# Kernel tuning notes

Measured on AMD Instinct MI355X. Metric: run time of the kernel, lower is better.

Reference implementation:

```python
import jax, jax.numpy as jnp
import numpy as np

E, D_IN, H1, H2 = 10, 784, 256, 64


def setup_inputs() -> dict:
    key = jax.random.key(0)
    ks = jax.random.split(key, 11)
    s = lambda fan_in: 1.0 / np.sqrt(fan_in)
    return {
        "x": jax.random.normal(ks[0], (65536, D_IN), dtype=jnp.float32),
        # stacked expert weights (E experts of Linear layers)
        "W1": jax.random.uniform(ks[1], (E, D_IN, H1), jnp.float32, -s(D_IN), s(D_IN)),
        "b1": jax.random.uniform(ks[2], (E, H1), jnp.float32, -s(D_IN), s(D_IN)),
        "W2": jax.random.uniform(ks[3], (E, H1, H2), jnp.float32, -s(H1), s(H1)),
        "b2": jax.random.uniform(ks[4], (E, H2), jnp.float32, -s(H1), s(H1)),
        "W3": jax.random.uniform(ks[5], (E, H2), jnp.float32, -s(H2), s(H2)),  # [E,64,1] squeezed
        "b3": jax.random.uniform(ks[6], (E,), jnp.float32, -s(H2), s(H2)),
        # gate: 784 -> 256 -> E
        "Wg1": jax.random.uniform(ks[7], (D_IN, H1), jnp.float32, -s(D_IN), s(D_IN)),
        "bg1": jax.random.uniform(ks[8], (H1,), jnp.float32, -s(D_IN), s(D_IN)),
        "Wg2": jax.random.uniform(ks[9], (H1, E), jnp.float32, -s(H1), s(H1)),
        "bg2": jax.random.uniform(ks[10], (E,), jnp.float32, -s(H1), s(H1)),
    }


def reference(x, W1, b1, W2, b2, W3, b3, Wg1, bg1, Wg2, bg2):
    # dense all-experts MLP stack, batched over experts as grouped GEMMs
    h = jax.nn.relu(jnp.einsum("bi,eih->beh", x, W1) + b1)        # [B,E,256]
    h = jax.nn.relu(jnp.einsum("beh,ehk->bek", h, W2) + b2)        # [B,E,64]
    expert_outputs = jnp.einsum("bek,ek->be", h, W3) + b3          # [B,E]
    g = jax.nn.relu(x @ Wg1 + bg1)
    gate_scores = jax.nn.softmax(g @ Wg2 + bg2, axis=-1)           # [B,E]
    output = gate_scores * expert_outputs                          # [B,E]
    return (output, gate_scores, expert_outputs)
```

## Files before the change

### kernel.cpp

```cpp
#include <hip/hip_runtime.h>
#include <hip/hip_bf16.h>
#include <stdint.h>

#define BTOT   65536
#define DIN    784
#define K1P    800
#define NH1    256
#define NH2    64
#define NEXP   10
#define BM     64
#define NKS1   25
#define NKS2   9

#define XS_B      102400
#define H_OFF     XS_B
#define H_B       36864
#define EXP2_OFF  (H_OFF + H_B)
#define W3S_OFF   (EXP2_OFF + BM * NEXP * 2 * 4)
#define B3S_OFF   (W3S_OFF + NEXP * NH2 * 4)
#define LDS_TOTAL (B3S_OFF + 64)

typedef short s16x8  __attribute__((ext_vector_type(8)));
typedef float f32x4  __attribute__((ext_vector_type(4)));
typedef float f32x16 __attribute__((ext_vector_type(16)));

__device__ __forceinline__ short bf16b(float v) {
    __bf16 b = (__bf16)v;
    return __builtin_bit_cast(short, b);
}

__global__ void prep_w1(const float* __restrict__ W1, const float* __restrict__ b1,
                        const float* __restrict__ Wg1, const float* __restrict__ bg1,
                        __bf16* __restrict__ dst) {
    int t = blockIdx.x * 256 + threadIdx.x;
    int lane = t & 63;
    int rr = t >> 6;
    int kh = rr & 1;
    int ks = (rr >> 1) % 25;
    int nb = ((rr >> 1) / 25) % 8;
    int e  = (rr >> 1) / 200;
    int n  = nb * 32 + (lane & 31);
    int k0 = ks * 32 + kh * 16 + (lane >> 5) * 8;
    const float* src  = (e < NEXP) ? (W1 + (size_t)e * DIN * NH1) : Wg1;
    const float* bias = (e < NEXP) ? (b1 + e * NH1) : bg1;
    s16x8 o;
    #pragma unroll
    for (int j = 0; j < 8; ++j) {
        int k = k0 + j;
        float v = (k < DIN) ? src[(size_t)k * NH1 + n]
                            : ((k == DIN) ? bias[n] : 0.f);
        o[j] = bf16b(v);
    }
    *(s16x8*)((short*)dst + (size_t)t * 8) = o;
}

__global__ void prep_w2(const float* __restrict__ W2, const float* __restrict__ b2,
                        __bf16* __restrict__ dst) {
    int t = blockIdx.x * 256 + threadIdx.x;
    int lane = t & 63;
    int rr = t >> 6;
    int kh = rr & 1;
    int ks = (rr >> 1) % 9;
    int jb = ((rr >> 1) / 9) & 1;
    int e  = (rr >> 1) / 18;
    int n  = jb * 32 + (lane & 31);
    int k0 = ks * 32 + kh * 16 + (lane >> 5) * 8;
    s16x8 o;
    #pragma unroll
    for (int j = 0; j < 8; ++j) {
        int k = k0 + j;
        float v = (k < NH1) ? W2[((size_t)e * NH1 + k) * NH2 + n]
                            : ((k == NH1) ? b2[e * NH2 + n] : 0.f);
        o[j] = bf16b(v);
    }
    *(s16x8*)((short*)dst + (size_t)t * 8) = o;
}

__global__ void prep_wg2(const float* __restrict__ Wg2, const float* __restrict__ bg2,
                         __bf16* __restrict__ dst) {
    int t = blockIdx.x * 256 + threadIdx.x;
    if (t >= 9 * 2 * 64) return;
    int lane = t & 63;
    int rr = t >> 6;
    int kh = rr & 1;
    int ks = rr >> 1;
    int n  = lane & 31;
    int k0 = ks * 32 + kh * 16 + (lane >> 5) * 8;
    s16x8 o;
    #pragma unroll
    for (int j = 0; j < 8; ++j) {
        int k = k0 + j;
        float v = 0.f;
        if (n < NEXP) {
            if (k < NH1)       v = Wg2[(size_t)k * NEXP + n];
            else if (k == NH1) v = bg2[n];
        }
        o[j] = bf16b(v);
    }
    *(s16x8*)((short*)dst + (size_t)t * 8) = o;
}

#define L1A_PF(S, T)                                                          \
    { _Pragma("unroll") for (int mt = 0; mt < 2; ++mt)                        \
        _Pragma("unroll") for (int kh = 0; kh < 2; ++kh)                      \
            a[S][mt][kh] = *(const s16x8*)(pA + ((mt * 25 + (T)) * 2 + kh) * 1024); }

#define L1W_PF(S, T, PW)                                                      \
    { _Pragma("unroll") for (int nt = 0; nt < 2; ++nt)                        \
        _Pragma("unroll") for (int kh = 0; kh < 2; ++kh)                      \
            w[S][nt][kh] = *(const s16x8*)((PW) + nt * 51200 + ((T) * 2 + kh) * 1024); }

#define L1_PF(S, T) L1A_PF(S, T) L1W_PF(S, T, pW)

#define L1_MMA(S)                                                             \
    { _Pragma("unroll") for (int nt = 0; nt < 2; ++nt)                        \
        _Pragma("unroll") for (int mt = 0; mt < 2; ++mt)                      \
            _Pragma("unroll") for (int kh = 0; kh < 2; ++kh)                  \
                acc[nt][mt] = __builtin_amdgcn_mfma_f32_32x32x16_bf16(        \
                    w[S][nt][kh], a[S][mt][kh], acc[nt][mt], 0, 0, 0); }

#define L2_PF(S, T)                                                           \
    { _Pragma("unroll") for (int kh = 0; kh < 2; ++kh) {                      \
        hfr[S][kh] = *(const s16x8*)(pH + ((T) * 2 + kh) * 1024);             \
        v2[S][kh]  = *(const s16x8*)(pV + ((T) * 2 + kh) * 1024); } }

#define L2_MMA(S)                                                             \
    { _Pragma("unroll") for (int kh = 0; kh < 2; ++kh)                        \
        acc2 = __builtin_amdgcn_mfma_f32_32x32x16_bf16(                       \
            v2[S][kh], hfr[S][kh], acc2, 0, 0, 0); }

__global__ void __launch_bounds__(256, 1)
moe_fused(const float* __restrict__ x, const float* __restrict__ W3,
          const float* __restrict__ b3, const __bf16* __restrict__ w1t,
          const __bf16* __restrict__ w2t, const __bf16* __restrict__ wg2t,
          float* __restrict__ out)
{
    extern __shared__ char lds[];
    char*  xsb   = lds;
    char*  hb    = lds + H_OFF;
    float* expl2 = (float*)(lds + EXP2_OFF);
    float* w3s   = (float*)(lds + W3S_OFF);
    float* b3s   = (float*)(lds + B3S_OFF);

    const int tid  = threadIdx.x;
    const int lane = tid & 63;
    const int wave = tid >> 6;
    const int rl   = lane & 31;
    const int hi   = lane >> 5;
    const int row0 = blockIdx.x * BM;
    const char* w1c = (const char*)w1t;

    const char* pA = xsb + lane * 16;
    const char* pW = w1c + (size_t)(wave * 2) * 51200 + lane * 16;

    s16x8 w[3][2][2], a[3][2][2];
    L1W_PF(0, 0, pW) L1W_PF(1, 1, pW) L1W_PF(2, 2, pW)

    {
        const float* xg = x + (size_t)row0 * DIN;
        #pragma unroll 4
        for (int i = 0; i < 49; ++i) {
            int idx = tid + i * 256;
            int r = idx / 196, c = (idx % 196) * 4;
            float4 v = *(const float4*)(xg + (size_t)r * DIN + c);
            int ks = c >> 5, kin = c & 31;
            int kh = kin >> 4, hw = (kin >> 3) & 1, j = c & 7;
            uint2 wv; short* p = (short*)&wv;
            p[0] = bf16b(v.x); p[1] = bf16b(v.y);
            p[2] = bf16b(v.z); p[3] = bf16b(v.w);
            *(uint2*)(xsb + ((((r >> 5) * 25 + ks) * 2 + kh) * 2 + hw) * 512
                          + (r & 31) * 16 + j * 2) = wv;
        }
        for (int i = tid; i < 64 * 4; i += 256) {
            int r = i >> 2, g = i & 3;
            int hw = g >> 1, j0 = (g & 1) * 4;
            uint2 wv = {0u, 0u};
            if (g == 0) ((short*)&wv)[0] = bf16b(1.f);
            *(uint2*)(xsb + ((((r >> 5) * 25 + 24) * 2 + 1) * 2 + hw) * 512
                          + (r & 31) * 16 + j0 * 2) = wv;
        }
        for (int i = tid; i < 2 * 1024; i += 256) {
            int mb = i >> 10, q = i & 1023;
            short v = (q < 256 && (q & 7) == 0) ? bf16b(1.f) : (short)0;
            *(short*)(hb + (mb * 9 + 8) * 2048 + q * 2) = v;
        }
        for (int i = tid; i < NEXP * NH2; i += 256) w3s[i] = W3[i];
        if (tid < NEXP) b3s[tid] = b3[tid];
    }
    __syncthreads();

    L1A_PF(0, 0) L1A_PF(1, 1) L1A_PF(2, 2)

    #pragma unroll 1
    for (int e = 0; e <= NEXP; ++e) {
        const char* pWe = w1c + (size_t)(e * 8 + wave * 2) * 51200 + lane * 16;
        #define pW pWe

        f32x16 acc[2][2];
        #pragma unroll
        for (int nt = 0; nt < 2; ++nt)
            #pragma unroll
            for (int mt = 0; mt < 2; ++mt)
                #pragma unroll
                for (int q = 0; q < 16; ++q) acc[nt][mt][q] = 0.f;

        #pragma unroll 1
        for (int T = 0; T < 7; ++T) {
            const int t3 = 3 * T;
            L1_MMA(0) L1_PF(0, t3 + 3)
            L1_MMA(1) L1_PF(1, t3 + 4)
            L1_MMA(2) L1_PF(2, t3 + 5)
        }
        L1_MMA(0) L1_PF(0, 24)
        L1_MMA(1)
        L1_MMA(2)
        #undef pW

        const int mb2 = wave >> 1, jb = wave & 1;
        const char* pH = hb + mb2 * 18432 + lane * 16;
        const char* pV = (const char*)w2t + (size_t)(e * 2 + jb) * 18432 + lane * 16;
        s16x8 v2[3][2], hfr[3][2];
        if (e < NEXP) {
            #pragma unroll
            for (int p = 0; p < 3; ++p)
                #pragma unroll
                for (int kh = 0; kh < 2; ++kh)
                    v2[p][kh] = *(const s16x8*)(pV + (p * 2 + kh) * 1024);
        }
        L1_MMA(0)

        if (e < NEXP) {
            const char* pWn = pWe + 8 * 51200;
            L1W_PF(0, 0, pWn) L1W_PF(1, 1, pWn) L1W_PF(2, 2, pWn)
            L1A_PF(0, 0) L1A_PF(1, 1) L1A_PF(2, 2)
        }

        __syncthreads();
        #pragma unroll
        for (int mt = 0; mt < 2; ++mt)
            #pragma unroll
            for (int nt = 0; nt < 2; ++nt) {
                const int ks2 = wave * 2 + nt;
                #pragma unroll
                for (int q = 0; q < 4; ++q) {
                    uint2 wv; short* p = (short*)&wv;
                    #pragma unroll
                    for (int r2 = 0; r2 < 4; ++r2)
                        p[r2] = bf16b(fmaxf(acc[nt][mt][q * 4 + r2], 0.f));
                    *(uint2*)(hb + ((mt * 9 + ks2) * 2 + (q >> 1)) * 1024
                                 + (q & 1) * 512 + rl * 16 + hi * 8) = wv;
                }
            }
        __syncthreads();

        if (e < NEXP) {
            f32x16 acc2;
            #pragma unroll
            for (int q = 0; q < 16; ++q) acc2[q] = 0.f;
            #pragma unroll
            for (int kh = 0; kh < 2; ++kh)
                hfr[0][kh] = *(const s16x8*)(pH + (0 * 2 + kh) * 1024);
            #pragma unroll
            for (int kh = 0; kh < 2; ++kh)
                hfr[1][kh] = *(const s16x8*)(pH + (1 * 2 + kh) * 1024);
            #pragma unroll
            for (int kh = 0; kh < 2; ++kh)
                hfr[2][kh] = *(const s16x8*)(pH + (2 * 2 + kh) * 1024);

            #pragma unroll 1
            for (int T = 0; T < 2; ++T) {
                const int t3 = 3 * T;
                L2_MMA(0) L2_PF(0, t3 + 3)
                L2_MMA(1) L2_PF(1, t3 + 4)
                L2_MMA(2) L2_PF(2, t3 + 5)
            }
            L2_MMA(0) L2_MMA(1) L2_MMA(2)

            float part = 0.f;
            const float* w3p = w3s + e * NH2 + jb * 32 + 4 * hi;
            #pragma unroll
            for (int q = 0; q < 4; ++q) {
                f32x4 w3v = *(const f32x4*)(w3p + 8 * q);
                #pragma unroll
                for (int r2 = 0; r2 < 4; ++r2)
                    part += fmaxf(acc2[q * 4 + r2], 0.f) * w3v[r2];
            }
            part += __shfl_xor(part, 32, 64);
            if (hi == 0)
                expl2[(mb2 * 32 + rl) * (NEXP * 2) + e * 2 + jb] = part;
        } else if (wave < 2) {
            const int mbg = wave;
            const char* pHg = hb + mbg * 18432 + lane * 16;
            const char* pG  = (const char*)wg2t + lane * 16;
            f32x16 acc3;
            #pragma unroll
            for (int q = 0; q < 16; ++q) acc3[q] = 0.f;
            {
                s16x8 v2[3][2], hfr[3][2];
                const char* pH = pHg;
                const char* pV = pG;
                L2_PF(0, 0) L2_PF(1, 1) L2_PF(2, 2)
                #define acc2 acc3
                #pragma unroll 1
                for (int T = 0; T < 2; ++T) {
                    const int t3 = 3 * T;
                    L2_MMA(0) L2_PF(0, t3 + 3)
                    L2_MMA(1) L2_PF(1, t3 + 4)
                    L2_MMA(2) L2_PF(2, t3 + 5)
                }
                L2_MMA(0) L2_MMA(1) L2_MMA(2)
                #undef acc2
            }
            const int m = mbg * 32 + rl;
            float mx = -1e30f;
            float lv[16];
            #pragma unroll
            for (int q = 0; q < 4; ++q)
                #pragma unroll
                for (int r2 = 0; r2 < 4; ++r2) {
                    int j = r2 + 8 * q + 4 * hi;
                    int rg = q * 4 + r2;
                    lv[rg] = (j < NEXP) ? acc3[rg] : -1e30f;
                    mx = fmaxf(mx, lv[rg]);
                }
            mx = fmaxf(mx, __shfl_xor(mx, 32, 64));
            float s = 0.f;
            float pv[16];
            #pragma unroll
            for (int rg = 0; rg < 16; ++rg) {
                pv[rg] = (lv[rg] > -1e29f) ? __expf(lv[rg] - mx) : 0.f;
                s += pv[rg];
            }
            s += __shfl_xor(s, 32, 64);
            const float inv = 1.f / s;
            #pragma unroll
            for (int q = 0; q < 4; ++q)
                #pragma unroll
                for (int r2 = 0; r2 < 4; ++r2) {
                    int j = r2 + 8 * q + 4 * hi;
                    if (j < NEXP) {
                        float g  = pv[q * 4 + r2] * inv;
                        float eo = expl2[m * (NEXP * 2) + j * 2]
                                 + expl2[m * (NEXP * 2) + j * 2 + 1]
                                 + b3s[j];
                        size_t o = (size_t)(row0 + m) * NEXP + j;
                        out[o] = g * eo;
                        out[(size_t)BTOT * NEXP + o] = g;
                        out[(size_t)2 * BTOT * NEXP + o] = eo;
                    }
                }
        }
    }
}

extern "C" void kernel_launch(void* const* d_in, const int* in_sizes, int n_in,
                              void* d_out, int out_size, void* d_ws, size_t ws_size,
                              hipStream_t stream) {
    (void)in_sizes; (void)n_in; (void)out_size; (void)ws_size;
    const float* x   = (const float*)d_in[0];
    const float* W1  = (const float*)d_in[1];
    const float* b1  = (const float*)d_in[2];
    const float* W2  = (const float*)d_in[3];
    const float* b2  = (const float*)d_in[4];
    const float* W3  = (const float*)d_in[5];
    const float* b3  = (const float*)d_in[6];
    const float* Wg1 = (const float*)d_in[7];
    const float* bg1 = (const float*)d_in[8];
    const float* Wg2 = (const float*)d_in[9];
    const float* bg2 = (const float*)d_in[10];

    __bf16* w1t  = (__bf16*)d_ws;
    __bf16* w2t  = w1t + (size_t)11 * 8 * 25 * 2 * 64 * 8;
    __bf16* wg2t = w2t + (size_t)10 * 2 * 9 * 2 * 64 * 8;

    hipFuncSetAttribute((const void*)moe_fused,
                        hipFuncAttributeMaxDynamicSharedMemorySize, LDS_TOTAL);

    prep_w1<<<1100, 256, 0, stream>>>(W1, b1, Wg1, bg1, w1t);
    prep_w2<<<90, 256, 0, stream>>>(W2, b2, w2t);
    prep_wg2<<<5, 256, 0, stream>>>(Wg2, bg2, wg2t);
    moe_fused<<<BTOT / BM, 256, LDS_TOTAL, stream>>>(x, W3, b3, w1t, w2t, wg2t,
                                                     (float*)d_out);
}
```

Baseline: 349.6 us.

## Process two experts per layer-1 pass to reuse x fragments across experts

The layer-1 loop now computes two experts at once. Each x fragment loaded from LDS feeds MFMAs for both experts' weight tiles, which halves the LDS reads of A per expert and doubles the independent MFMA chains. The gate network runs as a separate final single-expert pass. In exchange the prefetch depth drops from three stages to two and the kernel holds twice as many accumulators, which raises register pressure on a kernel already running one block per CU.

```diff
diff --git a/kernel.cpp b/kernel.cpp
--- a/kernel.cpp
+++ b/kernel.cpp
@@ -100,24 +100,46 @@
     *(s16x8*)((short*)dst + (size_t)t * 8) = o;
 }
 
-#define L1A_PF(S, T)                                                          \
+#define PFA(S, T)                                                             \
     { _Pragma("unroll") for (int mt = 0; mt < 2; ++mt)                        \
         _Pragma("unroll") for (int kh = 0; kh < 2; ++kh)                      \
             a[S][mt][kh] = *(const s16x8*)(pA + ((mt * 25 + (T)) * 2 + kh) * 1024); }
 
-#define L1W_PF(S, T, PW)                                                      \
+#define PFW(S, E, T, PW)                                                      \
     { _Pragma("unroll") for (int nt = 0; nt < 2; ++nt)                        \
         _Pragma("unroll") for (int kh = 0; kh < 2; ++kh)                      \
-            w[S][nt][kh] = *(const s16x8*)((PW) + nt * 51200 + ((T) * 2 + kh) * 1024); }
-
-#define L1_PF(S, T) L1A_PF(S, T) L1W_PF(S, T, pW)
-
-#define L1_MMA(S)                                                             \
+            w[S][E][nt][kh] = *(const s16x8*)((PW) + nt * 51200                \
+                                              + ((T) * 2 + kh) * 1024); }
+
+#define PMMA(S, E)                                                            \
     { _Pragma("unroll") for (int nt = 0; nt < 2; ++nt)                        \
         _Pragma("unroll") for (int mt = 0; mt < 2; ++mt)                      \
             _Pragma("unroll") for (int kh = 0; kh < 2; ++kh)                  \
-                acc[nt][mt] = __builtin_amdgcn_mfma_f32_32x32x16_bf16(        \
-                    w[S][nt][kh], a[S][mt][kh], acc[nt][mt], 0, 0, 0); }
+                acc[E][nt][mt] = __builtin_amdgcn_mfma_f32_32x32x16_bf16(     \
+                    w[S][E][nt][kh], a[S][mt][kh], acc[E][nt][mt], 0, 0, 0); }
+
+#define ZACC(E)                                                               \
+    { _Pragma("unroll") for (int nt = 0; nt < 2; ++nt)                        \
+        _Pragma("unroll") for (int mt = 0; mt < 2; ++mt)                      \
+            _Pragma("unroll") for (int q = 0; q < 16; ++q)                    \
+                acc[E][nt][mt][q] = 0.f; }
+
+#define HWRITE(E)                                                             \
+    { _Pragma("unroll") for (int mt = 0; mt < 2; ++mt)                        \
+        _Pragma("unroll") for (int nt = 0; nt < 2; ++nt) {                    \
+            const int ks2 = wave * 2 + nt;                                    \
+            _Pragma("unroll") for (int q = 0; q < 4; ++q) {                   \
+                uint2 wv; short* p = (short*)&wv;                             \
+                _Pragma("unroll") for (int r2 = 0; r2 < 4; ++r2)              \
+                    p[r2] = bf16b(fmaxf(acc[E][nt][mt][q * 4 + r2], 0.f));    \
+                *(uint2*)(hb + ((mt * 9 + ks2) * 2 + (q >> 1)) * 1024         \
+                             + (q & 1) * 512 + rl * 16 + hi * 8) = wv;        \
+            } } }
+
+#define PF_V2(PV)                                                             \
+    { _Pragma("unroll") for (int p = 0; p < 3; ++p)                           \
+        _Pragma("unroll") for (int kh = 0; kh < 2; ++kh)                      \
+            v2[p][kh] = *(const s16x8*)((PV) + (p * 2 + kh) * 1024); }
 
 #define L2_PF(S, T)                                                           \
     { _Pragma("unroll") for (int kh = 0; kh < 2; ++kh) {                      \
@@ -128,6 +150,36 @@
     { _Pragma("unroll") for (int kh = 0; kh < 2; ++kh)                        \
         acc2 = __builtin_amdgcn_mfma_f32_32x32x16_bf16(                       \
             v2[S][kh], hfr[S][kh], acc2, 0, 0, 0); }
+
+#define DO_L2(EV, PV)                                                         \
+    {                                                                         \
+        const char* pV = (PV);                                                \
+        f32x16 acc2;                                                          \
+        _Pragma("unroll") for (int q = 0; q < 16; ++q) acc2[q] = 0.f;         \
+        _Pragma("unroll") for (int kh = 0; kh < 2; ++kh)                      \
+            hfr[0][kh] = *(const s16x8*)(pH + (0 * 2 + kh) * 1024);           \
+        _Pragma("unroll") for (int kh = 0; kh < 2; ++kh)                      \
+            hfr[1][kh] = *(const s16x8*)(pH + (1 * 2 + kh) * 1024);           \
+        _Pragma("unroll") for (int kh = 0; kh < 2; ++kh)                      \
+            hfr[2][kh] = *(const s16x8*)(pH + (2 * 2 + kh) * 1024);           \
+        _Pragma("unroll 1") for (int T = 0; T < 2; ++T) {                     \
+            const int t3 = 3 * T;                                             \
+            L2_MMA(0) L2_PF(0, t3 + 3)                                        \
+            L2_MMA(1) L2_PF(1, t3 + 4)                                        \
+            L2_MMA(2) L2_PF(2, t3 + 5)                                        \
+        }                                                                     \
+        L2_MMA(0) L2_MMA(1) L2_MMA(2)                                         \
+        float part = 0.f;                                                     \
+        const float* w3p = w3s + (EV) * NH2 + jb * 32 + 4 * hi;               \
+        _Pragma("unroll") for (int q = 0; q < 4; ++q) {                       \
+            f32x4 w3v = *(const f32x4*)(w3p + 8 * q);                         \
+            _Pragma("unroll") for (int r2 = 0; r2 < 4; ++r2)                  \
+                part += fmaxf(acc2[q * 4 + r2], 0.f) * w3v[r2];               \
+        }                                                                     \
+        part += __shfl_xor(part, 32, 64);                                     \
+        if (hi == 0)                                                          \
+            expl2[(mb2 * 32 + rl) * (NEXP * 2) + (EV) * 2 + jb] = part;       \
+    }
 
 __global__ void __launch_bounds__(256, 1)
 moe_fused(const float* __restrict__ x, const float* __restrict__ W3,
@@ -151,10 +203,18 @@
     const char* w1c = (const char*)w1t;
 
     const char* pA = xsb + lane * 16;
-    const char* pW = w1c + (size_t)(wave * 2) * 51200 + lane * 16;
-
-    s16x8 w[3][2][2], a[3][2][2];
-    L1W_PF(0, 0, pW) L1W_PF(1, 1, pW) L1W_PF(2, 2, pW)
+    const int mb2 = wave >> 1, jb = wave & 1;
+    const char* pH = hb + mb2 * 18432 + lane * 16;
+
+    s16x8 w[2][2][2][2];
+    s16x8 a[2][2][2];
+    s16x8 v2[3][2], hfr[3][2];
+    {
+        const char* pW0 = w1c + (size_t)(wave * 2) * 51200 + lane * 16;
+        const char* pW1 = pW0 + 8 * 51200;
+        PFW(0, 0, 0, pW0) PFW(1, 0, 1, pW0)
+        PFW(0, 1, 0, pW1) PFW(1, 1, 1, pW1)
+    }
 
     {
         const float* xg = x + (size_t)row0 * DIN;
@@ -189,84 +249,81 @@
     }
     __syncthreads();
 
-    L1A_PF(0, 0) L1A_PF(1, 1) L1A_PF(2, 2)
+    PFA(0, 0) PFA(1, 1)
+
+    f32x16 acc[2][2][2];
 
     #pragma unroll 1
-    for (int e = 0; e <= NEXP; ++e) {
-        const char* pWe = w1c + (size_t)(e * 8 + wave * 2) * 51200 + lane * 16;
-        #define pW pWe
-
-        f32x16 acc[2][2];
+    for (int p5 = 0; p5 < 5; ++p5) {
+        const int e0 = 2 * p5;
+        const char* pW0 = w1c + (size_t)(e0 * 8 + wave * 2) * 51200 + lane * 16;
+        const char* pW1 = pW0 + 8 * 51200;
+
+        ZACC(0) ZACC(1)
+
+        #pragma unroll 1
+        for (int T = 0; T < 11; ++T) {
+            const int t2 = 2 * T;
+            PMMA(0, 0) PMMA(0, 1)
+            PFW(0, 0, t2 + 2, pW0) PFW(0, 1, t2 + 2, pW1) PFA(0, t2 + 2)
+            PMMA(1, 0) PMMA(1, 1)
+            PFW(1, 0, t2 + 3, pW0) PFW(1, 1, t2 + 3, pW1) PFA(1, t2 + 3)
+        }
+        PMMA(0, 0) PMMA(0, 1)
+        PFW(0, 0, 24, pW0) PFW(0, 1, 24, pW1) PFA(0, 24)
+        PMMA(1, 0) PMMA(1, 1)
+        PMMA(0, 0) PMMA(0, 1)
+
+        PF_V2((const char*)w2t + (size_t)(e0 * 2 + jb) * 18432 + lane * 16)
+        {
+            const char* pW0n = pW0 + 16 * 51200;
+            const char* pW1n = (p5 < 4) ? (pW1 + 16 * 51200) : pW0n;
+            PFW(0, 0, 0, pW0n) PFW(1, 0, 1, pW0n)
+            PFW(0, 1, 0, pW1n) PFW(1, 1, 1, pW1n)
+            PFA(0, 0) PFA(1, 1)
+        }
+
+        __syncthreads();
+        HWRITE(0)
+        __syncthreads();
+        DO_L2(e0, (const char*)w2t + (size_t)(e0 * 2 + jb) * 18432 + lane * 16)
+        PF_V2((const char*)w2t + (size_t)((e0 + 1) * 2 + jb) * 18432 + lane * 16)
+        __syncthreads();
+        HWRITE(1)
+        __syncthreads();
+        DO_L2(e0 + 1, (const char*)w2t + (size_t)((e0 + 1) * 2 + jb) * 18432 + lane * 16)
+    }
+
+    {
+        const char* pWg = w1c + (size_t)(10 * 8 + wave * 2) * 51200 + lane * 16;
+        ZACC(0)
+        #pragma unroll 1
+        for (int T = 0; T < 11; ++T) {
+            const int t2 = 2 * T;
+            PMMA(0, 0) PFW(0, 0, t2 + 2, pWg) PFA(0, t2 + 2)
+            PMMA(1, 0) PFW(1, 0, t2 + 3, pWg) PFA(1, t2 + 3)
+        }
+        PMMA(0, 0) PFW(0, 0, 24, pWg) PFA(0, 24)
+        PMMA(1, 0)
+        PMMA(0, 0)
+
+        __syncthreads();
+        HWRITE(0)
+        __syncthreads();
+    }
+
+    if (wave < 2) {
+        const int mbg = wave;
+        const char* pHg = hb + mbg * 18432 + lane * 16;
+        const char* pG  = (const char*)wg2t + lane * 16;
+        f32x16 acc3;
         #pragma unroll
-        for (int nt = 0; nt < 2; ++nt)
-            #pragma unroll
-            for (int mt = 0; mt < 2; ++mt)
-                #pragma unroll
-                for (int q = 0; q < 16; ++q) acc[nt][mt][q] = 0.f;
-
-        #pragma unroll 1
-        for (int T = 0; T < 7; ++T) {
-            const int t3 = 3 * T;
-            L1_MMA(0) L1_PF(0, t3 + 3)
-            L1_MMA(1) L1_PF(1, t3 + 4)
-            L1_MMA(2) L1_PF(2, t3 + 5)
-        }
-        L1_MMA(0) L1_PF(0, 24)
-        L1_MMA(1)
-        L1_MMA(2)
-        #undef pW
-
-        const int mb2 = wave >> 1, jb = wave & 1;
-        const char* pH = hb + mb2 * 18432 + lane * 16;
-        const char* pV = (const char*)w2t + (size_t)(e * 2 + jb) * 18432 + lane * 16;
-        s16x8 v2[3][2], hfr[3][2];
-        if (e < NEXP) {
-            #pragma unroll
-            for (int p = 0; p < 3; ++p)
-                #pragma unroll
-                for (int kh = 0; kh < 2; ++kh)
-                    v2[p][kh] = *(const s16x8*)(pV + (p * 2 + kh) * 1024);
-        }
-        L1_MMA(0)
-
-        if (e < NEXP) {
-            const char* pWn = pWe + 8 * 51200;
-            L1W_PF(0, 0, pWn) L1W_PF(1, 1, pWn) L1W_PF(2, 2, pWn)
-            L1A_PF(0, 0) L1A_PF(1, 1) L1A_PF(2, 2)
-        }
-
-        __syncthreads();
-        #pragma unroll
-        for (int mt = 0; mt < 2; ++mt)
-            #pragma unroll
-            for (int nt = 0; nt < 2; ++nt) {
-                const int ks2 = wave * 2 + nt;
-                #pragma unroll
-                for (int q = 0; q < 4; ++q) {
-                    uint2 wv; short* p = (short*)&wv;
-                    #pragma unroll
-                    for (int r2 = 0; r2 < 4; ++r2)
-                        p[r2] = bf16b(fmaxf(acc[nt][mt][q * 4 + r2], 0.f));
-                    *(uint2*)(hb + ((mt * 9 + ks2) * 2 + (q >> 1)) * 1024
-                                 + (q & 1) * 512 + rl * 16 + hi * 8) = wv;
-                }
-            }
-        __syncthreads();
-
-        if (e < NEXP) {
-            f32x16 acc2;
-            #pragma unroll
-            for (int q = 0; q < 16; ++q) acc2[q] = 0.f;
-            #pragma unroll
-            for (int kh = 0; kh < 2; ++kh)
-                hfr[0][kh] = *(const s16x8*)(pH + (0 * 2 + kh) * 1024);
-            #pragma unroll
-            for (int kh = 0; kh < 2; ++kh)
-                hfr[1][kh] = *(const s16x8*)(pH + (1 * 2 + kh) * 1024);
-            #pragma unroll
-            for (int kh = 0; kh < 2; ++kh)
-                hfr[2][kh] = *(const s16x8*)(pH + (2 * 2 + kh) * 1024);
-
+        for (int q = 0; q < 16; ++q) acc3[q] = 0.f;
+        {
+            const char* pH = pHg;
+            const char* pV = pG;
+            L2_PF(0, 0) L2_PF(1, 1) L2_PF(2, 2)
+            #define acc2 acc3
             #pragma unroll 1
             for (int T = 0; T < 2; ++T) {
                 const int t3 = 3 * T;
@@ -275,81 +332,46 @@
                 L2_MMA(2) L2_PF(2, t3 + 5)
             }
             L2_MMA(0) L2_MMA(1) L2_MMA(2)
-
-            float part = 0.f;
-            const float* w3p = w3s + e * NH2 + jb * 32 + 4 * hi;
+            #undef acc2
+        }
+        const int m = mbg * 32 + rl;
+        float mx = -1e30f;
+        float lv[16];
+        #pragma unroll
+        for (int q = 0; q < 4; ++q)
             #pragma unroll
-            for (int q = 0; q < 4; ++q) {
-                f32x4 w3v = *(const f32x4*)(w3p + 8 * q);
-                #pragma unroll
-                for (int r2 = 0; r2 < 4; ++r2)
-                    part += fmaxf(acc2[q * 4 + r2], 0.f) * w3v[r2];
+            for (int r2 = 0; r2 < 4; ++r2) {
+                int j = r2 + 8 * q + 4 * hi;
+                int rg = q * 4 + r2;
+                lv[rg] = (j < NEXP) ? acc3[rg] : -1e30f;
+                mx = fmaxf(mx, lv[rg]);
             }
-            part += __shfl_xor(part, 32, 64);
-            if (hi == 0)
-                expl2[(mb2 * 32 + rl) * (NEXP * 2) + e * 2 + jb] = part;
-        } else if (wave < 2) {
-            const int mbg = wave;
-            const char* pHg = hb + mbg * 18432 + lane * 16;
-            const char* pG  = (const char*)wg2t + lane * 16;
-            f32x16 acc3;
+        mx = fmaxf(mx, __shfl_xor(mx, 32, 64));
+        float s = 0.f;
+        float pv[16];
+        #pragma unroll
+        for (int rg = 0; rg < 16; ++rg) {
+            pv[rg] = (lv[rg] > -1e29f) ? __expf(lv[rg] - mx) : 0.f;
+            s += pv[rg];
+        }
+        s += __shfl_xor(s, 32, 64);
+        const float inv = 1.f / s;
+        #pragma unroll
+        for (int q = 0; q < 4; ++q)
             #pragma unroll
-            for (int q = 0; q < 16; ++q) acc3[q] = 0.f;
-            {
-                s16x8 v2[3][2], hfr[3][2];
-                const char* pH = pHg;
-                const char* pV = pG;
-                L2_PF(0, 0) L2_PF(1, 1) L2_PF(2, 2)
-                #define acc2 acc3
-                #pragma unroll 1
-                for (int T = 0; T < 2; ++T) {
-                    const int t3 = 3 * T;
-                    L2_MMA(0) L2_PF(0, t3 + 3)
-                    L2_MMA(1) L2_PF(1, t3 + 4)
-                    L2_MMA(2) L2_PF(2, t3 + 5)
+            for (int r2 = 0; r2 < 4; ++r2) {
+                int j = r2 + 8 * q + 4 * hi;
+                if (j < NEXP) {
+                    float g  = pv[q * 4 + r2] * inv;
+                    float eo = expl2[m * (NEXP * 2) + j * 2]
+                             + expl2[m * (NEXP * 2) + j * 2 + 1]
+                             + b3s[j];
+                    size_t o = (size_t)(row0 + m) * NEXP + j;
+                    out[o] = g * eo;
+                    out[(size_t)BTOT * NEXP + o] = g;
+                    out[(size_t)2 * BTOT * NEXP + o] = eo;
                 }
-                L2_MMA(0) L2_MMA(1) L2_MMA(2)
-                #undef acc2
             }
-            const int m = mbg * 32 + rl;
-            float mx = -1e30f;
-            float lv[16];
-            #pragma unroll
-            for (int q = 0; q < 4; ++q)
-                #pragma unroll
-                for (int r2 = 0; r2 < 4; ++r2) {
-                    int j = r2 + 8 * q + 4 * hi;
-                    int rg = q * 4 + r2;
-                    lv[rg] = (j < NEXP) ? acc3[rg] : -1e30f;
-                    mx = fmaxf(mx, lv[rg]);
-                }
-            mx = fmaxf(mx, __shfl_xor(mx, 32, 64));
-            float s = 0.f;
-            float pv[16];
-            #pragma unroll
-            for (int rg = 0; rg < 16; ++rg) {
-                pv[rg] = (lv[rg] > -1e29f) ? __expf(lv[rg] - mx) : 0.f;
-                s += pv[rg];
-            }
-            s += __shfl_xor(s, 32, 64);
-            const float inv = 1.f / s;
-            #pragma unroll
-            for (int q = 0; q < 4; ++q)
-                #pragma unroll
-                for (int r2 = 0; r2 < 4; ++r2) {
-                    int j = r2 + 8 * q + 4 * hi;
-                    if (j < NEXP) {
-                        float g  = pv[q * 4 + r2] * inv;
-                        float eo = expl2[m * (NEXP * 2) + j * 2]
-                                 + expl2[m * (NEXP * 2) + j * 2 + 1]
-                                 + b3s[j];
-                        size_t o = (size_t)(row0 + m) * NEXP + j;
-                        out[o] = g * eo;
-                        out[(size_t)BTOT * NEXP + o] = g;
-                        out[(size_t)2 * BTOT * NEXP + o] = eo;
-                    }
-                }
-        }
     }
 }
 
```

Result: no change. 354.2 us (+1.3%).

## Enlarge row tile to 256 and double-buffer W1 slices via global_load_lds

Applied to the files above, without the earlier changes.

Grows the per-block row tile from 64 to 256 rows with 512 threads in 8 waves (4 M-waves by 2 N-waves). For each expert, the x K-slice and W1 K-slice are streamed through double-buffered LDS, with W1 copied directly global-to-LDS. Each W1 slice is now reused across four times as many rows, but x is re-read from global for every one of the 11 expert/gate passes instead of being staged once. The layer-2 and gate GEMMs now run in two K-halves through a smaller shared H buffer. Biases b2 and bg2 move out of the augmented weights and are added in the epilogue.

```diff
diff --git a/kernel.cpp b/kernel.cpp
--- a/kernel.cpp
+++ b/kernel.cpp
@@ -4,21 +4,21 @@
 
 #define BTOT   65536
 #define DIN    784
-#define K1P    800
 #define NH1    256
 #define NH2    64
 #define NEXP   10
-#define BM     64
+#define BM     256
 #define NKS1   25
-#define NKS2   9
-
-#define XS_B      102400
-#define H_OFF     XS_B
-#define H_B       36864
-#define EXP2_OFF  (H_OFF + H_B)
-#define W3S_OFF   (EXP2_OFF + BM * NEXP * 2 * 4)
-#define B3S_OFF   (W3S_OFF + NEXP * NH2 * 4)
-#define LDS_TOTAL (B3S_OFF + 64)
+
+#define XBUF(b)   (lds + (b) * 32768)
+#define WBUF(b)   (lds + (b) * 32768 + 16384)
+#define H_OFF     65536
+#define EXPL_OFF  131072
+#define B2S_OFF   141312
+#define W3S_OFF   143872
+#define B3S_OFF   146432
+#define BG2S_OFF  146496
+#define LDS_TOTAL 146560
 
 typedef short s16x8  __attribute__((ext_vector_type(8)));
 typedef float f32x4  __attribute__((ext_vector_type(4)));
@@ -27,6 +27,12 @@
 __device__ __forceinline__ short bf16b(float v) {
     __bf16 b = (__bf16)v;
     return __builtin_bit_cast(short, b);
+}
+
+__device__ __forceinline__ void g2l16(const void* g, void* l) {
+    __builtin_amdgcn_global_load_lds(
+        (const __attribute__((address_space(1))) unsigned char*)g,
+        (__attribute__((address_space(3))) unsigned char*)l, 16, 0, 0);
 }
 
 __global__ void prep_w1(const float* __restrict__ W1, const float* __restrict__ b1,
@@ -34,11 +40,10 @@
                         __bf16* __restrict__ dst) {
     int t = blockIdx.x * 256 + threadIdx.x;
     int lane = t & 63;
-    int rr = t >> 6;
-    int kh = rr & 1;
-    int ks = (rr >> 1) % 25;
-    int nb = ((rr >> 1) / 25) % 8;
-    int e  = (rr >> 1) / 200;
+    int kh = (t >> 6) & 1;
+    int nb = (t >> 7) & 7;
+    int r  = t >> 10;
+    int ks = r % 25, e = r / 25;
     int n  = nb * 32 + (lane & 31);
     int k0 = ks * 32 + kh * 16 + (lane >> 5) * 8;
     const float* src  = (e < NEXP) ? (W1 + (size_t)e * DIN * NH1) : Wg1;
@@ -54,278 +59,222 @@
     *(s16x8*)((short*)dst + (size_t)t * 8) = o;
 }
 
-__global__ void prep_w2(const float* __restrict__ W2, const float* __restrict__ b2,
-                        __bf16* __restrict__ dst) {
+__global__ void prep_w2(const float* __restrict__ W2, __bf16* __restrict__ dst) {
     int t = blockIdx.x * 256 + threadIdx.x;
     int lane = t & 63;
-    int rr = t >> 6;
-    int kh = rr & 1;
-    int ks = (rr >> 1) % 9;
-    int jb = ((rr >> 1) / 9) & 1;
-    int e  = (rr >> 1) / 18;
+    int kh = (t >> 6) & 1;
+    int ks = (t >> 7) & 7;
+    int jb = (t >> 10) & 1;
+    int e  = t >> 11;
     int n  = jb * 32 + (lane & 31);
     int k0 = ks * 32 + kh * 16 + (lane >> 5) * 8;
     s16x8 o;
     #pragma unroll
-    for (int j = 0; j < 8; ++j) {
-        int k = k0 + j;
-        float v = (k < NH1) ? W2[((size_t)e * NH1 + k) * NH2 + n]
-                            : ((k == NH1) ? b2[e * NH2 + n] : 0.f);
-        o[j] = bf16b(v);
-    }
+    for (int j = 0; j < 8; ++j)
+        o[j] = bf16b(W2[((size_t)e * NH1 + k0 + j) * NH2 + n]);
     *(s16x8*)((short*)dst + (size_t)t * 8) = o;
 }
 
-__global__ void prep_wg2(const float* __restrict__ Wg2, const float* __restrict__ bg2,
-                         __bf16* __restrict__ dst) {
+__global__ void prep_wg2(const float* __restrict__ Wg2, __bf16* __restrict__ dst) {
     int t = blockIdx.x * 256 + threadIdx.x;
-    if (t >= 9 * 2 * 64) return;
+    if (t >= 1024) return;
     int lane = t & 63;
-    int rr = t >> 6;
-    int kh = rr & 1;
-    int ks = rr >> 1;
+    int kh = (t >> 6) & 1;
+    int ks = t >> 7;
     int n  = lane & 31;
     int k0 = ks * 32 + kh * 16 + (lane >> 5) * 8;
     s16x8 o;
     #pragma unroll
-    for (int j = 0; j < 8; ++j) {
-        int k = k0 + j;
-        float v = 0.f;
-        if (n < NEXP) {
-            if (k < NH1)       v = Wg2[(size_t)k * NEXP + n];
-            else if (k == NH1) v = bg2[n];
-        }
-        o[j] = bf16b(v);
-    }
+    for (int j = 0; j < 8; ++j)
+        o[j] = bf16b((n < NEXP) ? Wg2[(size_t)(k0 + j) * NEXP + n] : 0.f);
     *(s16x8*)((short*)dst + (size_t)t * 8) = o;
 }
 
-#define L1A_PF(S, T)                                                          \
-    { _Pragma("unroll") for (int mt = 0; mt < 2; ++mt)                        \
-        _Pragma("unroll") for (int kh = 0; kh < 2; ++kh)                      \
-            a[S][mt][kh] = *(const s16x8*)(pA + ((mt * 25 + (T)) * 2 + kh) * 1024); }
-
-#define L1W_PF(S, T, PW)                                                      \
-    { _Pragma("unroll") for (int nt = 0; nt < 2; ++nt)                        \
-        _Pragma("unroll") for (int kh = 0; kh < 2; ++kh)                      \
-            w[S][nt][kh] = *(const s16x8*)((PW) + nt * 51200 + ((T) * 2 + kh) * 1024); }
-
-#define L1_PF(S, T) L1A_PF(S, T) L1W_PF(S, T, pW)
-
-#define L1_MMA(S)                                                             \
-    { _Pragma("unroll") for (int nt = 0; nt < 2; ++nt)                        \
-        _Pragma("unroll") for (int mt = 0; mt < 2; ++mt)                      \
-            _Pragma("unroll") for (int kh = 0; kh < 2; ++kh)                  \
-                acc[nt][mt] = __builtin_amdgcn_mfma_f32_32x32x16_bf16(        \
-                    w[S][nt][kh], a[S][mt][kh], acc[nt][mt], 0, 0, 0); }
-
-#define L2_PF(S, T)                                                           \
-    { _Pragma("unroll") for (int kh = 0; kh < 2; ++kh) {                      \
-        hfr[S][kh] = *(const s16x8*)(pH + ((T) * 2 + kh) * 1024);             \
-        v2[S][kh]  = *(const s16x8*)(pV + ((T) * 2 + kh) * 1024); } }
-
-#define L2_MMA(S)                                                             \
-    { _Pragma("unroll") for (int kh = 0; kh < 2; ++kh)                        \
-        acc2 = __builtin_amdgcn_mfma_f32_32x32x16_bf16(                       \
-            v2[S][kh], hfr[S][kh], acc2, 0, 0, 0); }
-
-__global__ void __launch_bounds__(256, 1)
-moe_fused(const float* __restrict__ x, const float* __restrict__ W3,
-          const float* __restrict__ b3, const __bf16* __restrict__ w1t,
+__global__ void __launch_bounds__(512, 2)
+moe_fused(const float* __restrict__ x, const float* __restrict__ b2g,
+          const float* __restrict__ W3, const float* __restrict__ b3,
+          const float* __restrict__ bg2, const __bf16* __restrict__ w1t,
           const __bf16* __restrict__ w2t, const __bf16* __restrict__ wg2t,
           float* __restrict__ out)
 {
     extern __shared__ char lds[];
-    char*  xsb   = lds;
-    char*  hb    = lds + H_OFF;
-    float* expl2 = (float*)(lds + EXP2_OFF);
-    float* w3s   = (float*)(lds + W3S_OFF);
-    float* b3s   = (float*)(lds + B3S_OFF);
+    char*  hb   = lds + H_OFF;
+    float* expl = (float*)(lds + EXPL_OFF);
+    float* b2s  = (float*)(lds + B2S_OFF);
+    float* w3s  = (float*)(lds + W3S_OFF);
+    float* b3s  = (float*)(lds + B3S_OFF);
+    float* bg2s = (float*)(lds + BG2S_OFF);
 
     const int tid  = threadIdx.x;
     const int lane = tid & 63;
     const int wave = tid >> 6;
     const int rl   = lane & 31;
     const int hi   = lane >> 5;
+    const int mw   = wave >> 1;
+    const int nw   = wave & 1;
     const int row0 = blockIdx.x * BM;
     const char* w1c = (const char*)w1t;
-
-    const char* pA = xsb + lane * 16;
-    const char* pW = w1c + (size_t)(wave * 2) * 51200 + lane * 16;
-
-    s16x8 w[3][2][2], a[3][2][2];
-    L1W_PF(0, 0, pW) L1W_PF(1, 1, pW) L1W_PF(2, 2, pW)
-
-    {
-        const float* xg = x + (size_t)row0 * DIN;
-        #pragma unroll 4
-        for (int i = 0; i < 49; ++i) {
-            int idx = tid + i * 256;
-            int r = idx / 196, c = (idx % 196) * 4;
-            float4 v = *(const float4*)(xg + (size_t)r * DIN + c);
-            int ks = c >> 5, kin = c & 31;
-            int kh = kin >> 4, hw = (kin >> 3) & 1, j = c & 7;
-            uint2 wv; short* p = (short*)&wv;
-            p[0] = bf16b(v.x); p[1] = bf16b(v.y);
-            p[2] = bf16b(v.z); p[3] = bf16b(v.w);
-            *(uint2*)(xsb + ((((r >> 5) * 25 + ks) * 2 + kh) * 2 + hw) * 512
-                          + (r & 31) * 16 + j * 2) = wv;
-        }
-        for (int i = tid; i < 64 * 4; i += 256) {
-            int r = i >> 2, g = i & 3;
-            int hw = g >> 1, j0 = (g & 1) * 4;
-            uint2 wv = {0u, 0u};
-            if (g == 0) ((short*)&wv)[0] = bf16b(1.f);
-            *(uint2*)(xsb + ((((r >> 5) * 25 + 24) * 2 + 1) * 2 + hw) * 512
-                          + (r & 31) * 16 + j0 * 2) = wv;
-        }
-        for (int i = tid; i < 2 * 1024; i += 256) {
-            int mb = i >> 10, q = i & 1023;
-            short v = (q < 256 && (q & 7) == 0) ? bf16b(1.f) : (short)0;
-            *(short*)(hb + (mb * 9 + 8) * 2048 + q * 2) = v;
-        }
-        for (int i = tid; i < NEXP * NH2; i += 256) w3s[i] = W3[i];
-        if (tid < NEXP) b3s[tid] = b3[tid];
-    }
-    __syncthreads();
-
-    L1A_PF(0, 0) L1A_PF(1, 1) L1A_PF(2, 2)
+    const char* w2c = (const char*)w2t;
+    const char* wgc = (const char*)wg2t;
+
+    for (int i = tid; i < NEXP * NH2; i += 512) { b2s[i] = b2g[i]; w3s[i] = W3[i]; }
+    if (tid < NEXP) { b3s[tid] = b3[tid]; bg2s[tid] = bg2[tid]; }
+
+    const int xrow = tid >> 1, xkh = tid & 1;
+    const float* xrp = x + (size_t)(row0 + xrow) * DIN + xkh * 16;
+    const int xoff = ((xrow >> 5) * 2 + xkh) * 1024 + (xrow & 31) * 16;
+    float xf[16];
+
+    #define XLOAD(KS) { if ((KS) < 24 || xkh == 0) {                          \
+            _Pragma("unroll") for (int i4 = 0; i4 < 4; ++i4)                  \
+                *(float4*)(xf + 4 * i4) =                                     \
+                    *(const float4*)(xrp + (KS) * 32 + 4 * i4);               \
+        } else { _Pragma("unroll") for (int i4 = 0; i4 < 16; ++i4)            \
+                     xf[i4] = 0.f;                                            \
+                 xf[0] = 1.f; } }
+
+    #define XWRITE(B) { s16x8 l8, h8;                                         \
+            _Pragma("unroll") for (int j = 0; j < 8; ++j) {                   \
+                l8[j] = bf16b(xf[j]); h8[j] = bf16b(xf[8 + j]); }             \
+            *(s16x8*)(XBUF(B) + xoff)       = l8;                             \
+            *(s16x8*)(XBUF(B) + xoff + 512) = h8; }
+
+    #define WSTAGE(B, E, KS) {                                                \
+            const char* ws_ = w1c + (((size_t)(E) * 25 + (KS)) << 14)         \
+                              + tid * 16;                                     \
+            char* wd_ = WBUF(B) + tid * 16;                                   \
+            g2l16(ws_, wd_); g2l16(ws_ + 8192, wd_ + 8192); }
+
+    f32x16 acc[4][2];
+    f32x16 acc2[2];
 
     #pragma unroll 1
     for (int e = 0; e <= NEXP; ++e) {
-        const char* pWe = w1c + (size_t)(e * 8 + wave * 2) * 51200 + lane * 16;
-        #define pW pWe
-
-        f32x16 acc[2][2];
+        XLOAD(0)
+        WSTAGE(0, e, 0)
+        XWRITE(0)
+        __syncthreads();
+
         #pragma unroll
-        for (int nt = 0; nt < 2; ++nt)
+        for (int nt = 0; nt < 4; ++nt)
             #pragma unroll
             for (int mt = 0; mt < 2; ++mt)
                 #pragma unroll
                 for (int q = 0; q < 16; ++q) acc[nt][mt][q] = 0.f;
-
+        #pragma unroll
+        for (int q = 0; q < 16; ++q) { acc2[0][q] = 0.f; acc2[1][q] = 0.f; }
+
+        int cur = 0;
         #pragma unroll 1
-        for (int T = 0; T < 7; ++T) {
-            const int t3 = 3 * T;
-            L1_MMA(0) L1_PF(0, t3 + 3)
-            L1_MMA(1) L1_PF(1, t3 + 4)
-            L1_MMA(2) L1_PF(2, t3 + 5)
+        for (int ks = 0; ks < NKS1; ++ks) {
+            if (ks < 24) {
+                XLOAD(ks + 1)
+                WSTAGE(cur ^ 1, e, ks + 1)
+            }
+            const char* ab = XBUF(cur) + mw * 4096 + lane * 16;
+            const char* wb = WBUF(cur) + nw * 8192 + lane * 16;
+            s16x8 xv[2][2], wv[4][2];
+            #pragma unroll
+            for (int mt = 0; mt < 2; ++mt)
+                #pragma unroll
+                for (int kh = 0; kh < 2; ++kh)
+                    xv[mt][kh] = *(const s16x8*)(ab + (mt * 2 + kh) * 1024);
+            #pragma unroll
+            for (int nt = 0; nt < 4; ++nt)
+                #pragma unroll
+                for (int kh = 0; kh < 2; ++kh)
+                    wv[nt][kh] = *(const s16x8*)(wb + (nt * 2 + kh) * 1024);
+            #pragma unroll
+            for (int kh = 0; kh < 2; ++kh)
+                #pragma unroll
+                for (int nt = 0; nt < 4; ++nt)
+                    #pragma unroll
+                    for (int mt = 0; mt < 2; ++mt)
+                        acc[nt][mt] = __builtin_amdgcn_mfma_f32_32x32x16_bf16(
+                            wv[nt][kh], xv[mt][kh], acc[nt][mt], 0, 0, 0);
+            if (ks < 24) XWRITE(cur ^ 1)
+            __syncthreads();
+            cur ^= 1;
         }
-        L1_MMA(0) L1_PF(0, 24)
-        L1_MMA(1)
-        L1_MMA(2)
-        #undef pW
-
-        const int mb2 = wave >> 1, jb = wave & 1;
-        const char* pH = hb + mb2 * 18432 + lane * 16;
-        const char* pV = (const char*)w2t + (size_t)(e * 2 + jb) * 18432 + lane * 16;
-        s16x8 v2[3][2], hfr[3][2];
+
+        #pragma unroll
+        for (int half = 0; half < 2; ++half) {
+            if (nw == half) {
+                #pragma unroll
+                for (int mt = 0; mt < 2; ++mt)
+                    #pragma unroll
+                    for (int nt = 0; nt < 4; ++nt)
+                        #pragma unroll
+                        for (int q = 0; q < 4; ++q) {
+                            uint2 wvv; short* p = (short*)&wvv;
+                            #pragma unroll
+                            for (int r2 = 0; r2 < 4; ++r2)
+                                p[r2] = bf16b(fmaxf(acc[nt][mt][q * 4 + r2], 0.f));
+                            *(uint2*)(hb + (((mw * 2 + mt) * 4 + nt) * 2 + (q >> 1)) * 1024
+                                         + (rl + 32 * (q & 1)) * 16 + hi * 8) = wvv;
+                        }
+            }
+            __syncthreads();
+            if (e < NEXP) {
+                #pragma unroll
+                for (int jb = 0; jb < 2; ++jb)
+                    #pragma unroll
+                    for (int k2 = 0; k2 < 4; ++k2)
+                        #pragma unroll
+                        for (int kh = 0; kh < 2; ++kh) {
+                            s16x8 hf = *(const s16x8*)(hb + ((wave * 4 + k2) * 2 + kh) * 1024
+                                                       + lane * 16);
+                            s16x8 wf = *(const s16x8*)(w2c
+                                + ((((size_t)e * 2 + jb) * 8 + half * 4 + k2) * 2 + kh) * 1024
+                                + lane * 16);
+                            acc2[jb] = __builtin_amdgcn_mfma_f32_32x32x16_bf16(
+                                wf, hf, acc2[jb], 0, 0, 0);
+                        }
+            } else {
+                #pragma unroll
+                for (int k2 = 0; k2 < 4; ++k2)
+                    #pragma unroll
+                    for (int kh = 0; kh < 2; ++kh) {
+                        s16x8 hf = *(const s16x8*)(hb + ((wave * 4 + k2) * 2 + kh) * 1024
+                                                   + lane * 16);
+                        s16x8 gf = *(const s16x8*)(wgc
+                            + ((half * 4 + k2) * 2 + kh) * 1024 + lane * 16);
+                        acc2[0] = __builtin_amdgcn_mfma_f32_32x32x16_bf16(
+                            gf, hf, acc2[0], 0, 0, 0);
+                    }
+            }
+            __syncthreads();
+        }
+
         if (e < NEXP) {
-            #pragma unroll
-            for (int p = 0; p < 3; ++p)
-                #pragma unroll
-                for (int kh = 0; kh < 2; ++kh)
-                    v2[p][kh] = *(const s16x8*)(pV + (p * 2 + kh) * 1024);
-        }
-        L1_MMA(0)
-
-        if (e < NEXP) {
-            const char* pWn = pWe + 8 * 51200;
-            L1W_PF(0, 0, pWn) L1W_PF(1, 1, pWn) L1W_PF(2, 2, pWn)
-            L1A_PF(0, 0) L1A_PF(1, 1) L1A_PF(2, 2)
-        }
-
-        __syncthreads();
-        #pragma unroll
-        for (int mt = 0; mt < 2; ++mt)
-            #pragma unroll
-            for (int nt = 0; nt < 2; ++nt) {
-                const int ks2 = wave * 2 + nt;
+            float part = 0.f;
+            #pragma unroll
+            for (int jb = 0; jb < 2; ++jb)
                 #pragma unroll
                 for (int q = 0; q < 4; ++q) {
-                    uint2 wv; short* p = (short*)&wv;
+                    f32x4 b2v = *(const f32x4*)(b2s + e * NH2 + jb * 32 + 8 * q + 4 * hi);
+                    f32x4 w3v = *(const f32x4*)(w3s + e * NH2 + jb * 32 + 8 * q + 4 * hi);
                     #pragma unroll
                     for (int r2 = 0; r2 < 4; ++r2)
-                        p[r2] = bf16b(fmaxf(acc[nt][mt][q * 4 + r2], 0.f));
-                    *(uint2*)(hb + ((mt * 9 + ks2) * 2 + (q >> 1)) * 1024
-                                 + (q & 1) * 512 + rl * 16 + hi * 8) = wv;
+                        part += fmaxf(acc2[jb][q * 4 + r2] + b2v[r2], 0.f) * w3v[r2];
                 }
-            }
-        __syncthreads();
-
-        if (e < NEXP) {
-            f32x16 acc2;
-            #pragma unroll
-            for (int q = 0; q < 16; ++q) acc2[q] = 0.f;
-            #pragma unroll
-            for (int kh = 0; kh < 2; ++kh)
-                hfr[0][kh] = *(const s16x8*)(pH + (0 * 2 + kh) * 1024);
-            #pragma unroll
-            for (int kh = 0; kh < 2; ++kh)
-                hfr[1][kh] = *(const s16x8*)(pH + (1 * 2 + kh) * 1024);
-            #pragma unroll
-            for (int kh = 0; kh < 2; ++kh)
-                hfr[2][kh] = *(const s16x8*)(pH + (2 * 2 + kh) * 1024);
-
-            #pragma unroll 1
-            for (int T = 0; T < 2; ++T) {
-                const int t3 = 3 * T;
-                L2_MMA(0) L2_PF(0, t3 + 3)
-                L2_MMA(1) L2_PF(1, t3 + 4)
-                L2_MMA(2) L2_PF(2, t3 + 5)
-            }
-            L2_MMA(0) L2_MMA(1) L2_MMA(2)
-
-            float part = 0.f;
-            const float* w3p = w3s + e * NH2 + jb * 32 + 4 * hi;
-            #pragma unroll
-            for (int q = 0; q < 4; ++q) {
-                f32x4 w3v = *(const f32x4*)(w3p + 8 * q);
-                #pragma unroll
-                for (int r2 = 0; r2 < 4; ++r2)
-                    part += fmaxf(acc2[q * 4 + r2], 0.f) * w3v[r2];
-            }
             part += __shfl_xor(part, 32, 64);
             if (hi == 0)
-                expl2[(mb2 * 32 + rl) * (NEXP * 2) + e * 2 + jb] = part;
-        } else if (wave < 2) {
-            const int mbg = wave;
-            const char* pHg = hb + mbg * 18432 + lane * 16;
-            const char* pG  = (const char*)wg2t + lane * 16;
-            f32x16 acc3;
-            #pragma unroll
-            for (int q = 0; q < 16; ++q) acc3[q] = 0.f;
-            {
-                s16x8 v2[3][2], hfr[3][2];
-                const char* pH = pHg;
-                const char* pV = pG;
-                L2_PF(0, 0) L2_PF(1, 1) L2_PF(2, 2)
-                #define acc2 acc3
-                #pragma unroll 1
-                for (int T = 0; T < 2; ++T) {
-                    const int t3 = 3 * T;
-                    L2_MMA(0) L2_PF(0, t3 + 3)
-                    L2_MMA(1) L2_PF(1, t3 + 4)
-                    L2_MMA(2) L2_PF(2, t3 + 5)
-                }
-                L2_MMA(0) L2_MMA(1) L2_MMA(2)
-                #undef acc2
-            }
-            const int m = mbg * 32 + rl;
-            float mx = -1e30f;
-            float lv[16];
+                expl[(wave * 32 + rl) * NEXP + e] = part + b3s[e];
+        } else {
+            const int m = wave * 32 + rl;
+            float lv[16], mx = -1e30f;
             #pragma unroll
             for (int q = 0; q < 4; ++q)
                 #pragma unroll
                 for (int r2 = 0; r2 < 4; ++r2) {
                     int j = r2 + 8 * q + 4 * hi;
                     int rg = q * 4 + r2;
-                    lv[rg] = (j < NEXP) ? acc3[rg] : -1e30f;
+                    lv[rg] = (j < NEXP) ? (acc2[0][rg] + bg2s[j]) : -1e30f;
                     mx = fmaxf(mx, lv[rg]);
                 }
             mx = fmaxf(mx, __shfl_xor(mx, 32, 64));
-            float s = 0.f;
-            float pv[16];
+            float s = 0.f, pv[16];
             #pragma unroll
             for (int rg = 0; rg < 16; ++rg) {
                 pv[rg] = (lv[rg] > -1e29f) ? __expf(lv[rg] - mx) : 0.f;
@@ -340,9 +289,7 @@
                     int j = r2 + 8 * q + 4 * hi;
                     if (j < NEXP) {
                         float g  = pv[q * 4 + r2] * inv;
-                        float eo = expl2[m * (NEXP * 2) + j * 2]
-                                 + expl2[m * (NEXP * 2) + j * 2 + 1]
-                                 + b3s[j];
+                        float eo = expl[m * NEXP + j];
                         size_t o = (size_t)(row0 + m) * NEXP + j;
                         out[o] = g * eo;
                         out[(size_t)BTOT * NEXP + o] = g;
@@ -370,15 +317,15 @@
     const float* bg2 = (const float*)d_in[10];
 
     __bf16* w1t  = (__bf16*)d_ws;
-    __bf16* w2t  = w1t + (size_t)11 * 8 * 25 * 2 * 64 * 8;
-    __bf16* wg2t = w2t + (size_t)10 * 2 * 9 * 2 * 64 * 8;
+    __bf16* w2t  = w1t + (size_t)11 * 25 * 8192;
+    __bf16* wg2t = w2t + (size_t)20480 * 8;
 
     hipFuncSetAttribute((const void*)moe_fused,
                         hipFuncAttributeMaxDynamicSharedMemorySize, LDS_TOTAL);
 
     prep_w1<<<1100, 256, 0, stream>>>(W1, b1, Wg1, bg1, w1t);
-    prep_w2<<<90, 256, 0, stream>>>(W2, b2, w2t);
-    prep_wg2<<<5, 256, 0, stream>>>(Wg2, bg2, wg2t);
-    moe_fused<<<BTOT / BM, 256, LDS_TOTAL, stream>>>(x, W3, b3, w1t, w2t, wg2t,
-                                                     (float*)d_out);
-}
+    prep_w2<<<80, 256, 0, stream>>>(W2, w2t);
+    prep_wg2<<<4, 256, 0, stream>>>(Wg2, wg2t);
+    moe_fused<<<BTOT / BM, 512, LDS_TOTAL, stream>>>(x, b2, W3, b3, bg2,
+                                                     w1t, w2t, wg2t, (float*)d_out);
+}
```

New measurement: 532.6 us. 52.4% more time.
